# Kernel optimization log

Hardware: AMD Instinct MI355X
Metric: run time of the kernel (lower is better)

## Reference

```python
import jax, jax.numpy as jnp
import numpy as np

N = 50000; E = 800000; NFEAT = 128; NHID = 64; CONCAT = 2; NCLASS = 40
D = CONCAT * NHID
BN_EPS = 1e-5


def setup_inputs() -> dict:
    key = jax.random.key(0)
    ks = jax.random.split(key, 16)
    rn = lambda k, s, sc=0.05: jax.random.normal(k, s, jnp.float32) * sc
    return {
        "x1a": rn(ks[0], (N, NFEAT), 1.0),
        "x1b": rn(ks[1], (N, NFEAT), 1.0),
        "x2a": rn(ks[2], (N, NFEAT), 1.0),
        "x2b": rn(ks[3], (N, NFEAT), 1.0),
        "edge_index1": jax.random.randint(ks[4], (2, E), 0, N),
        "edge_index2": jax.random.randint(ks[5], (2, E), 0, N),
        "Wi": rn(ks[6], (CONCAT, NFEAT, NHID)),
        "bi": jnp.zeros((CONCAT, NHID), jnp.float32),
        "gi": jnp.ones((CONCAT, NHID), jnp.float32),
        "bei": jnp.zeros((CONCAT, NHID), jnp.float32),
        "Wm": rn(ks[7], (2, D, D)),
        "bm": jnp.zeros((2, D), jnp.float32),
        "gm": jnp.ones((2, D), jnp.float32),
        "bem": jnp.zeros((2, D), jnp.float32),
        "Wf": rn(ks[8], (D, NCLASS)),
        "bf": jnp.zeros((NCLASS,), jnp.float32),
        "fc1w1_W": rn(ks[9], (D,)),
        "fc1w1_b": jnp.zeros((1,), jnp.float32),
        "fc1w2_W": rn(ks[10], (D,)),
        "fc1w2_b": jnp.zeros((1,), jnp.float32),
        "aws_w1_W": rn(ks[11], (2, D)),
        "aws_w1_b": jnp.zeros((2,), jnp.float32),
        "aws_w2_W": rn(ks[12], (2, D)),
        "aws_w2_b": jnp.zeros((2,), jnp.float32),
        "fcw1_W": rn(ks[13], (NCLASS,)),
        "fcw1_b": jnp.zeros((1,), jnp.float32),
        "fcw2_W": rn(ks[14], (NCLASS,)),
        "fcw2_b": jnp.zeros((1,), jnp.float32),
    }


def _gcn_norm(edge_index, n):
    # GCN symmetric normalization with self-loops (cached=True behaviour)
    loop = jnp.arange(n)
    src = jnp.concatenate([edge_index[0], loop])
    dst = jnp.concatenate([edge_index[1], loop])
    deg = jax.ops.segment_sum(jnp.ones_like(dst, jnp.float32), dst, n)
    dinv = jnp.where(deg > 0, deg ** -0.5, 0.0)
    return src, dst, dinv[src] * dinv[dst]


def _gcn(x, W, b, g):
    # GCNConv: dense projection then sparse scatter-based aggregation
    src, dst, norm = g
    h = x @ W
    agg = jax.ops.segment_sum(h[src] * norm[:, None], dst, x.shape[0])
    return agg + b


def _bn(x, gamma, beta):
    m = x.mean(0)
    v = jnp.mean((x - m) ** 2, axis=0)
    return (x - m) * jax.lax.rsqrt(v + BN_EPS) * gamma + beta


def _gate(x1, x2, w1, b1, w2, b2):
    # sigmoid gates L1-normalized; only the last node's row is used (w[-1,:])
    s1 = jax.nn.sigmoid(jnp.dot(x1[-1], w1) + b1)
    s2 = jax.nn.sigmoid(jnp.dot(x2[-1], w2) + b2)
    t = s1 + s2
    return s1 / t, s2 / t


def _forward(x1a, x1b, x2a, x2b, g1, g2, Wi, bi, gi, bei, Wm, bm, gm, bem,
             Wf, bf, fc1w1_W, fc1w1_b, fc1w2_W, fc1w2_b,
             aws_w1_W, aws_w1_b, aws_w2_W, aws_w2_b,
             fcw1_W, fcw1_b, fcw2_W, fcw2_b):
    xs1, xs2 = (x1a, x1b), (x2a, x2b)
    h1 = jnp.concatenate([jax.nn.relu(_bn(_gcn(xs1[i], Wi[i], bi[i], g1), gi[i], bei[i]))
                          for i in range(CONCAT)], axis=-1)
    h2 = jnp.concatenate([jax.nn.relu(_bn(_gcn(xs2[i], Wi[i], bi[i], g2), gi[i], bei[i]))
                          for i in range(CONCAT)], axis=-1)
    w1, w2 = _gate(h1, h2, fc1w1_W, fc1w1_b[0], fc1w2_W, fc1w2_b[0])
    x = w1 * h1 + w2 * h2
    for i in range(Wm.shape[0]):  # middle layers (n_layers - 2)
        a = jax.nn.relu(_bn(_gcn(x, Wm[i], bm[i], g1), gm[i], bem[i]))
        b = jax.nn.relu(_bn(_gcn(x, Wm[i], bm[i], g2), gm[i], bem[i]))
        w1, w2 = _gate(a, b, aws_w1_W[i], aws_w1_b[i], aws_w2_W[i], aws_w2_b[i])
        x = w1 * a + w2 * b
    p1 = _gcn(x, Wf, bf, g1)
    p2 = _gcn(x, Wf, bf, g2)
    w1, w2 = _gate(p1, p2, fcw1_W, fcw1_b[0], fcw2_W, fcw2_b[0])
    return (w1 * p1 + w2 * p2, p1, p2)


def reference(x1a, x1b, x2a, x2b, edge_index1, edge_index2, Wi, bi, gi, bei,
              Wm, bm, gm, bem, Wf, bf, fc1w1_W, fc1w1_b, fc1w2_W, fc1w2_b,
              aws_w1_W, aws_w1_b, aws_w2_W, aws_w2_b,
              fcw1_W, fcw1_b, fcw2_W, fcw2_b):
    g1 = _gcn_norm(edge_index1, N)
    g2 = _gcn_norm(edge_index2, N)
    return _forward(x1a, x1b, x2a, x2b, g1, g2, Wi, bi, gi, bei, Wm, bm, gm, bem,
                    Wf, bf, fc1w1_W, fc1w1_b, fc1w2_W, fc1w2_b,
                    aws_w1_W, aws_w1_b, aws_w2_W, aws_w2_b,
                    fcw1_W, fcw1_b, fcw2_W, fcw2_b)
```

## Files before the change

### kernel.cpp

```cpp
#include <hip/hip_runtime.h>
#include <hip/hip_fp16.h>


#define DFEAT 128

typedef __attribute__((ext_vector_type(8))) short bf16x8;
typedef __attribute__((ext_vector_type(4))) float f32x4;

__device__ __forceinline__ unsigned short f2bf(float f) {
    unsigned u = __float_as_uint(f);
    u += 0x7fffu + ((u >> 16) & 1u);
    return (unsigned short)(u >> 16);
}
__device__ __forceinline__ float bf2f(unsigned short u) {
    return __uint_as_float((unsigned)u << 16);
}
__device__ __forceinline__ float4 bf4tof4(ushort4 u) {
    return make_float4(__uint_as_float((unsigned)u.x << 16),
                       __uint_as_float((unsigned)u.y << 16),
                       __uint_as_float((unsigned)u.z << 16),
                       __uint_as_float((unsigned)u.w << 16));
}
__device__ __forceinline__ unsigned f2h16(float f) {
    return (unsigned)__half_as_ushort(__float2half(f));
}
__device__ __forceinline__ float h16f(unsigned u) {
    return __half2float(__ushort_as_half((unsigned short)u));
}

constexpr int RSH = 13;
constexpr int RSZ = 8192;
constexpr int NRMAX = 8;
constexpr int EPA = 2048;
constexpr int SUBS = 16;
constexpr int SCAP = 160000;

__global__ __launch_bounds__(256) void partA_kernel(
    const int* __restrict__ src1, const int* __restrict__ dst1,
    const int* __restrict__ src2, const int* __restrict__ dst2,
    int* __restrict__ stg, int* __restrict__ gcount, int E, int nr) {
    int g = blockIdx.y;
    const int* src = g ? src2 : src1;
    const int* dst = g ? dst2 : dst1;
    __shared__ int buf[EPA];
    __shared__ int buf2[EPA];
    __shared__ int cnt8[NRMAX + 1], pre8[NRMAX + 1], base8[NRMAX];
    int t = threadIdx.x;
    if (t < NRMAX) cnt8[t] = 0;
    __syncthreads();
    int e0 = blockIdx.x * EPA;
    int e1 = min(e0 + EPA, E);
    int ec = e1 - e0;
    for (int i = e0 + t; i < e1; i += 256) {
        int d = dst[i];
        int s = src[i];
        buf[i - e0] = (d << 16) | s;
        atomicAdd(&cnt8[d >> RSH], 1);
    }
    __syncthreads();
    if (t == 0) {
        int run = 0;
        for (int r = 0; r < nr; ++r) { pre8[r] = run; run += cnt8[r]; }
        pre8[nr] = run;
    }
    __syncthreads();
    if (t < nr) {
        base8[t] = atomicAdd(&gcount[g * NRMAX + t], cnt8[t]);
        cnt8[t] = 0;
    }
    __syncthreads();
    for (int j = t; j < ec; j += 256) {
        int v = buf[j];
        int d = (unsigned)v >> 16;
        int r = d >> RSH;
        int p = pre8[r] + atomicAdd(&cnt8[r], 1);
        buf2[p] = ((d & (RSZ - 1)) << 16) | (v & 0xFFFF);
    }
    __syncthreads();
    for (int j = t; j < ec; j += 256) {
        int r = 0;
        while (j >= pre8[r + 1]) ++r;
        int gpos = base8[r] + (j - pre8[r]);
        if (gpos < SCAP) stg[((size_t)g * NRMAX + r) * SCAP + gpos] = buf2[j];
    }
}

__global__ __launch_bounds__(256) void histB_kernel(
    const int* __restrict__ stg, const int* __restrict__ gcount,
    int* __restrict__ baseB, int nr) {
    int g = blockIdx.y;
    int r = blockIdx.x / SUBS;
    int sub = blockIdx.x % SUBS;
    __shared__ int hist[RSZ];
    int t = threadIdx.x;
    for (int i = t; i < RSZ; i += 256) hist[i] = 0;
    __syncthreads();
    int len = min(gcount[g * NRMAX + r], SCAP);
    int seg = (len + SUBS - 1) / SUBS;
    int e0 = sub * seg, e1 = min(e0 + seg, len);
    const int* sp = stg + ((size_t)g * NRMAX + r) * SCAP;
    for (int i = e0 + t; i < e1; i += 256) atomicAdd(&hist[(unsigned)sp[i] >> 16], 1);
    __syncthreads();
    int* bp = baseB + (((size_t)(g * NRMAX + r) * SUBS + sub) << RSH);
    for (int i = t; i < RSZ; i += 256) bp[i] = hist[i];
}

__global__ __launch_bounds__(256) void scanB_kernel(
    int* __restrict__ baseB, int* __restrict__ cnt1, int* __restrict__ cnt2, int n) {
    int node = blockIdx.x * 256 + threadIdx.x;
    int g = blockIdx.y;
    if (node >= n) return;
    int r = node >> RSH, dloc = node & (RSZ - 1);
    int* p = baseB + (((size_t)(g * NRMAX + r) * SUBS) << RSH) + dloc;
    int run = 0;
#pragma unroll
    for (int s = 0; s < SUBS; ++s) {
        int v = p[(size_t)s << RSH];
        p[(size_t)s << RSH] = run;
        run += v;
    }
    (g ? cnt2 : cnt1)[node] = run;
}

__global__ __launch_bounds__(256) void fillC_kernel(
    const int* __restrict__ stg, const int* __restrict__ gcount,
    const int* __restrict__ baseB,
    const int* __restrict__ rp1, const int* __restrict__ rp2,
    const float* __restrict__ dv1, const float* __restrict__ dv2,
    int* __restrict__ cs1, int* __restrict__ cs2, int n, int nr) {
    int g = blockIdx.y;
    int r = blockIdx.x / SUBS;
    int sub = blockIdx.x % SUBS;
    const int* rp = g ? rp2 : rp1;
    const float* dv = g ? dv2 : dv1;
    int* cs = g ? cs2 : cs1;
    __shared__ int off[RSZ];
    int t = threadIdx.x;
    int r0 = r << RSH;
    int rn = min(RSZ, n - r0);
    if (rn <= 0) return;
    const int* bp = baseB + (((size_t)(g * NRMAX + r) * SUBS + sub) << RSH);
    for (int i = t; i < rn; i += 256) off[i] = bp[i] + rp[r0 + i];
    __syncthreads();
    int len = min(gcount[g * NRMAX + r], SCAP);
    int seg = (len + SUBS - 1) / SUBS;
    int e0 = sub * seg, e1 = min(e0 + seg, len);
    const int* sp = stg + ((size_t)g * NRMAX + r) * SCAP;
    for (int i = e0 + t; i < e1; i += 256) {
        int v = sp[i];
        int dloc = (unsigned)v >> 16;
        int s = v & 0xFFFF;
        float w = dv[r0 + dloc] * dv[s];
        int pos = atomicAdd(&off[dloc], 1);
        cs[pos] = (int)((f2h16(w) << 16) | (unsigned)s);
    }
}

__global__ __launch_bounds__(256) void blocksum_kernel(const int* __restrict__ c1,
                                                       const int* __restrict__ c2,
                                                       int* __restrict__ bs, int n, int nb) {
    const int* c = blockIdx.y ? c2 : c1;
    int* out = bs + (size_t)blockIdx.y * nb;
    int t = threadIdx.x;
    int base = blockIdx.x * 2048 + t * 8;
    int s = 0;
#pragma unroll
    for (int i = 0; i < 8; ++i) {
        int idx = base + i;
        if (idx < n) s += c[idx];
    }
    __shared__ int red[256];
    red[t] = s;
    __syncthreads();
    for (int o = 128; o > 0; o >>= 1) {
        if (t < o) red[t] += red[t + o];
        __syncthreads();
    }
    if (t == 0) out[blockIdx.x] = red[0];
}

__global__ void scansums_kernel(int* __restrict__ bs, int nb, int* __restrict__ rp1,
                                int* __restrict__ rp2, int n, int E, float* __restrict__ stats) {
    int t = threadIdx.x;
    if (t < 2) {
        int* b = bs + (size_t)t * nb;
        int run = 0;
        for (int i = 0; i < nb; ++i) {
            int v = b[i];
            b[i] = run;
            run += v;
        }
        (t ? rp2 : rp1)[n] = E;
    }
    for (int i = t; i < 512; i += 64) stats[i] = 0.f;
}

__global__ __launch_bounds__(256) void writerp_kernel(const int* __restrict__ c1,
                                                      const int* __restrict__ c2,
                                                      const int* __restrict__ bs,
                                                      int* __restrict__ rp1, int* __restrict__ rp2,
                                                      float* __restrict__ dv1,
                                                      float* __restrict__ dv2, int n, int nb) {
    const int* c = blockIdx.y ? c2 : c1;
    int* rp = blockIdx.y ? rp2 : rp1;
    float* dv = blockIdx.y ? dv2 : dv1;
    int boff = bs[(size_t)blockIdx.y * nb + blockIdx.x];
    int t = threadIdx.x;
    int base = blockIdx.x * 2048 + t * 8;
    int v[8];
    int s = 0;
#pragma unroll
    for (int i = 0; i < 8; ++i) {
        int idx = base + i;
        v[i] = (idx < n) ? c[idx] : 0;
        s += v[i];
    }
    __shared__ int red[256];
    red[t] = s;
    __syncthreads();
    for (int o = 1; o < 256; o <<= 1) {
        int x = (t >= o) ? red[t - o] : 0;
        __syncthreads();
        red[t] += x;
        __syncthreads();
    }
    int run = boff + red[t] - s;
#pragma unroll
    for (int i = 0; i < 8; ++i) {
        int idx = base + i;
        if (idx < n) {
            rp[idx] = run;
            dv[idx] = rsqrtf((float)(v[i] + 1));
            run += v[i];
        }
    }
}

template <int FV, typename OutT>
__global__ __launch_bounds__(256) void dualagg_kernel(
    const unsigned short* __restrict__ h1, const unsigned short* __restrict__ h2,
    const int* __restrict__ rp1, const int* __restrict__ cs1, const float* __restrict__ dv1,
    const int* __restrict__ rp2, const int* __restrict__ cs2, const float* __restrict__ dv2,
    const float* __restrict__ bias, OutT* __restrict__ o1, OutT* __restrict__ o2, int n) {
    constexpr int COLS = FV * 4;
    const unsigned short* h;
    const int *rp, *cs;
    const float* dv;
    OutT* out;
    if (blockIdx.y == 0) { h = h1; rp = rp1; cs = cs1; dv = dv1; out = o1; }
    else                 { h = h2; rp = rp2; cs = cs2; dv = dv2; out = o2; }
    int wid = blockIdx.x * 4 + (threadIdx.x >> 6);
    if (wid >= n) return;
    int lane = threadIdx.x & 63;
    int half = lane >> 5;
    int l = lane & 31;
    bool act = (l < FV);
    float4 acc = make_float4(0.f, 0.f, 0.f, 0.f);
    int e0 = rp[wid], e1 = rp[wid + 1];
    int e = e0 + half;
    for (; e + 6 < e1; e += 8) {
        int va = cs[e], vb = cs[e + 2], vc = cs[e + 4], vd = cs[e + 6];
        float wa = h16f((unsigned)va >> 16); int sa = va & 0xFFFF;
        float wb = h16f((unsigned)vb >> 16); int sb = vb & 0xFFFF;
        float wc = h16f((unsigned)vc >> 16); int sc = vc & 0xFFFF;
        float wd = h16f((unsigned)vd >> 16); int sd = vd & 0xFFFF;
        if (act) {
            float4 ha = bf4tof4(((const ushort4*)(h + (size_t)sa * COLS))[l]);
            float4 hb = bf4tof4(((const ushort4*)(h + (size_t)sb * COLS))[l]);
            float4 hc = bf4tof4(((const ushort4*)(h + (size_t)sc * COLS))[l]);
            float4 hd = bf4tof4(((const ushort4*)(h + (size_t)sd * COLS))[l]);
            acc.x = fmaf(wa, ha.x, acc.x); acc.y = fmaf(wa, ha.y, acc.y);
            acc.z = fmaf(wa, ha.z, acc.z); acc.w = fmaf(wa, ha.w, acc.w);
            acc.x = fmaf(wb, hb.x, acc.x); acc.y = fmaf(wb, hb.y, acc.y);
            acc.z = fmaf(wb, hb.z, acc.z); acc.w = fmaf(wb, hb.w, acc.w);
            acc.x = fmaf(wc, hc.x, acc.x); acc.y = fmaf(wc, hc.y, acc.y);
            acc.z = fmaf(wc, hc.z, acc.z); acc.w = fmaf(wc, hc.w, acc.w);
            acc.x = fmaf(wd, hd.x, acc.x); acc.y = fmaf(wd, hd.y, acc.y);
            acc.z = fmaf(wd, hd.z, acc.z); acc.w = fmaf(wd, hd.w, acc.w);
        }
    }
    for (; e < e1; e += 2) {
        int va = cs[e];
        float wa = h16f((unsigned)va >> 16); int sa = va & 0xFFFF;
        if (act) {
            float4 ha = bf4tof4(((const ushort4*)(h + (size_t)sa * COLS))[l]);
            acc.x = fmaf(wa, ha.x, acc.x); acc.y = fmaf(wa, ha.y, acc.y);
            acc.z = fmaf(wa, ha.z, acc.z); acc.w = fmaf(wa, ha.w, acc.w);
        }
    }
    acc.x += __shfl_xor(acc.x, 32);
    acc.y += __shfl_xor(acc.y, 32);
    acc.z += __shfl_xor(acc.z, 32);
    acc.w += __shfl_xor(acc.w, 32);
    if (half == 0 && act) {
        float dn = dv[wid];
        float w = dn * dn;
        float4 hv = bf4tof4(((const ushort4*)(h + (size_t)wid * COLS))[l]);
        acc.x = fmaf(w, hv.x, acc.x); acc.y = fmaf(w, hv.y, acc.y);
        acc.z = fmaf(w, hv.z, acc.z); acc.w = fmaf(w, hv.w, acc.w);
        float4 b = ((const float4*)bias)[l];
        acc.x += b.x; acc.y += b.y; acc.z += b.z; acc.w += b.w;
        if constexpr (sizeof(OutT) == 4) {
            ((float4*)((float*)out + (size_t)wid * COLS))[l] = acc;
        } else {
            ushort4 o;
            o.x = f2bf(acc.x); o.y = f2bf(acc.y); o.z = f2bf(acc.z); o.w = f2bf(acc.w);
            ((ushort4*)((unsigned short*)out + (size_t)wid * COLS))[l] = o;
        }
    }
}

__global__ __launch_bounds__(256) void gemm_l1_kernel(
    const float* __restrict__ x1a, const float* __restrict__ x1b, const float* __restrict__ x2a,
    const float* __restrict__ x2b, const float* __restrict__ Wi, unsigned short* __restrict__ H1,
    unsigned short* __restrict__ H2, int nrows) {
    constexpr int CG = 16;
    const float* X = (blockIdx.y == 0) ? x1a : (blockIdx.y == 1) ? x1b
                     : (blockIdx.y == 2) ? x2a : x2b;
    const float* W = Wi + (blockIdx.y & 1) * 128 * 64;
    unsigned short* Y = (blockIdx.y < 2) ? H1 : H2;
    int ocol = (int)(blockIdx.y & 1) * 64;
    __shared__ float Ws[32][64];
    __shared__ float Xs[64][32];
    int tid = threadIdx.x;
    int row0 = blockIdx.x * 64;
    int cg = tid % CG;
    int rg = tid / CG;
    float4 acc[4];
#pragma unroll
    for (int i = 0; i < 4; ++i) acc[i] = make_float4(0.f, 0.f, 0.f, 0.f);
    for (int kc = 0; kc < 4; ++kc) {
        for (int i = tid; i < 32 * CG; i += 256) {
            int r = i / CG, c = i % CG;
            *(float4*)&Ws[r][c * 4] = *(const float4*)(W + (size_t)(kc * 32 + r) * 64 + c * 4);
        }
        for (int i = tid; i < 64 * 8; i += 256) {
            int r = i / 8, c = i % 8;
            int gr = row0 + r;
            float4 v = make_float4(0.f, 0.f, 0.f, 0.f);
            if (gr < nrows) v = *(const float4*)(X + (size_t)gr * DFEAT + kc * 32 + c * 4);
            *(float4*)&Xs[r][c * 4] = v;
        }
        __syncthreads();
#pragma unroll
        for (int k = 0; k < 32; ++k) {
            float4 w = *(float4*)&Ws[k][cg * 4];
#pragma unroll
            for (int i = 0; i < 4; ++i) {
                float a = Xs[rg * 4 + i][k];
                acc[i].x = fmaf(a, w.x, acc[i].x);
                acc[i].y = fmaf(a, w.y, acc[i].y);
                acc[i].z = fmaf(a, w.z, acc[i].z);
                acc[i].w = fmaf(a, w.w, acc[i].w);
            }
        }
        __syncthreads();
    }
#pragma unroll
    for (int i = 0; i < 4; ++i) {
        int r = row0 + rg * 4 + i;
        if (r < nrows) {
            ushort4 o;
            o.x = f2bf(acc[i].x); o.y = f2bf(acc[i].y);
            o.z = f2bf(acc[i].z); o.w = f2bf(acc[i].w);
            *(ushort4*)(Y + (size_t)r * DFEAT + ocol + cg * 4) = o;
        }
    }
}

__global__ __launch_bounds__(256) void prepW_kernel(const float* __restrict__ Wm,
                                                    unsigned short* __restrict__ Wt) {
    int o = blockIdx.x * 256 + threadIdx.x;
    int l = blockIdx.y;
    int kk = o & 31;
    int col = (o >> 5) & 127;
    int kc = o >> 12;
    int k = kc * 32 + kk;
    Wt[(size_t)l * 16384 + o] = f2bf(Wm[(size_t)l * 16384 + (size_t)k * 128 + col]);
}

__global__ __launch_bounds__(256) void gemm_mfma_kernel(
    const unsigned short* __restrict__ Abf, const unsigned short* __restrict__ Bbf,
    const float* __restrict__ ss, const float* __restrict__ wout,
    const unsigned short* __restrict__ Wt, unsigned short* __restrict__ Y, int nrows) {
    __shared__ short Xs[64][128];
    int tid = threadIdx.x;
    int row0 = blockIdx.x * 64;
    int wave = tid >> 6, lane = tid & 63;
    int m = lane & 15, quad = lane >> 4;
    float w1 = wout[0], w2 = wout[1];
    for (int u = tid; u < 1024; u += 256) {
        int r = u >> 4;
        int col0 = (u & 15) * 8;
        int gr = row0 + r;
        if (gr < nrows) {
#pragma unroll
            for (int hh = 0; hh < 2; ++hh) {
                int c = col0 + hh * 4;
                float4 fa = bf4tof4(*(const ushort4*)(Abf + (size_t)gr * 128 + c));
                float4 fb = bf4tof4(*(const ushort4*)(Bbf + (size_t)gr * 128 + c));
                float4 sa = *(const float4*)(ss + c);
                float4 ha = *(const float4*)(ss + 128 + c);
                float4 sb = *(const float4*)(ss + 256 + c);
                float4 hb = *(const float4*)(ss + 384 + c);
                ushort4 o;
                o.x = f2bf(w1 * fmaxf(fmaf(fa.x, sa.x, ha.x), 0.f) +
                           w2 * fmaxf(fmaf(fb.x, sb.x, hb.x), 0.f));
                o.y = f2bf(w1 * fmaxf(fmaf(fa.y, sa.y, ha.y), 0.f) +
                           w2 * fmaxf(fmaf(fb.y, sb.y, hb.y), 0.f));
                o.z = f2bf(w1 * fmaxf(fmaf(fa.z, sa.z, ha.z), 0.f) +
                           w2 * fmaxf(fmaf(fb.z, sb.z, hb.z), 0.f));
                o.w = f2bf(w1 * fmaxf(fmaf(fa.w, sa.w, ha.w), 0.f) +
                           w2 * fmaxf(fmaf(fb.w, sb.w, hb.w), 0.f));
                *(ushort4*)&Xs[r][c] = o;
            }
        } else {
            ushort4 z = {0, 0, 0, 0};
            *(ushort4*)&Xs[r][col0] = z;
            *(ushort4*)&Xs[r][col0 + 4] = z;
        }
    }
    __syncthreads();
    f32x4 acc[8];
#pragma unroll
    for (int i = 0; i < 8; ++i) acc[i] = (f32x4){0.f, 0.f, 0.f, 0.f};
#pragma unroll
    for (int kc = 0; kc < 4; ++kc) {
        bf16x8 a = *(const bf16x8*)&Xs[wave * 16 + m][kc * 32 + quad * 8];
#pragma unroll
        for (int ct = 0; ct < 8; ++ct) {
            const short* bp = (const short*)(Wt + ((size_t)(kc * 128 + ct * 16 + m) * 32) + quad * 8);
            bf16x8 b = *(const bf16x8*)bp;
            acc[ct] = __builtin_amdgcn_mfma_f32_16x16x32_bf16(a, b, acc[ct], 0, 0, 0);
        }
    }
#pragma unroll
    for (int ct = 0; ct < 8; ++ct) {
#pragma unroll
        for (int i = 0; i < 4; ++i) {
            int gr = row0 + wave * 16 + quad * 4 + i;
            if (gr < nrows) Y[(size_t)gr * 128 + ct * 16 + m] = f2bf(acc[ct][i]);
        }
    }
}

template <int CG, int RPT>
__global__ __launch_bounds__(256) void gemm_fused_kernel(
    const unsigned short* __restrict__ Abf, const unsigned short* __restrict__ Bbf,
    const float* __restrict__ ss, const float* __restrict__ wout, const float* __restrict__ W,
    unsigned short* __restrict__ Y, int nrows, int fout, int ostride) {
    __shared__ float Ws[32][CG * 4];
    __shared__ float Xs[64][32];
    int tid = threadIdx.x;
    int row0 = blockIdx.x * 64;
    int cg = tid % CG;
    int rg = tid / CG;
    float w1 = wout[0], w2 = wout[1];
    float4 acc[RPT];
#pragma unroll
    for (int i = 0; i < RPT; ++i) acc[i] = make_float4(0.f, 0.f, 0.f, 0.f);
    for (int kc = 0; kc < 4; ++kc) {
        for (int i = tid; i < 32 * CG; i += 256) {
            int r = i / CG, c = i % CG;
            float4 w;
            if ((c * 4 + 3) < fout) {
                w = *(const float4*)(W + (size_t)(kc * 32 + r) * fout + c * 4);
            } else {
                float t0 = (c * 4 + 0) < fout ? W[(size_t)(kc * 32 + r) * fout + c * 4 + 0] : 0.f;
                float t1 = (c * 4 + 1) < fout ? W[(size_t)(kc * 32 + r) * fout + c * 4 + 1] : 0.f;
                float t2 = (c * 4 + 2) < fout ? W[(size_t)(kc * 32 + r) * fout + c * 4 + 2] : 0.f;
                float t3 = (c * 4 + 3) < fout ? W[(size_t)(kc * 32 + r) * fout + c * 4 + 3] : 0.f;
                w = make_float4(t0, t1, t2, t3);
            }
            *(float4*)&Ws[r][c * 4] = w;
        }
        for (int i = tid; i < 64 * 8; i += 256) {
            int r = i / 8, c = i % 8;
            int gr = row0 + r;
            int col0 = kc * 32 + c * 4;
            float4 v = make_float4(0.f, 0.f, 0.f, 0.f);
            if (gr < nrows) {
                float4 a = bf4tof4(*(const ushort4*)(Abf + (size_t)gr * DFEAT + col0));
                float4 b = bf4tof4(*(const ushort4*)(Bbf + (size_t)gr * DFEAT + col0));
                float4 scA = *(const float4*)(ss + col0);
                float4 shA = *(const float4*)(ss + DFEAT + col0);
                float4 scB = *(const float4*)(ss + 2 * DFEAT + col0);
                float4 shB = *(const float4*)(ss + 3 * DFEAT + col0);
                v.x = w1 * fmaxf(fmaf(a.x, scA.x, shA.x), 0.f) +
                      w2 * fmaxf(fmaf(b.x, scB.x, shB.x), 0.f);
                v.y = w1 * fmaxf(fmaf(a.y, scA.y, shA.y), 0.f) +
                      w2 * fmaxf(fmaf(b.y, scB.y, shB.y), 0.f);
                v.z = w1 * fmaxf(fmaf(a.z, scA.z, shA.z), 0.f) +
                      w2 * fmaxf(fmaf(b.z, scB.z, shB.z), 0.f);
                v.w = w1 * fmaxf(fmaf(a.w, scA.w, shA.w), 0.f) +
                      w2 * fmaxf(fmaf(b.w, scB.w, shB.w), 0.f);
            }
            *(float4*)&Xs[r][c * 4] = v;
        }
        __syncthreads();
#pragma unroll
        for (int k = 0; k < 32; ++k) {
            float4 w = *(float4*)&Ws[k][cg * 4];
#pragma unroll
            for (int i = 0; i < RPT; ++i) {
                float a = Xs[rg * RPT + i][k];
                acc[i].x = fmaf(a, w.x, acc[i].x);
                acc[i].y = fmaf(a, w.y, acc[i].y);
                acc[i].z = fmaf(a, w.z, acc[i].z);
                acc[i].w = fmaf(a, w.w, acc[i].w);
            }
        }
        __syncthreads();
    }
    if (cg * 4 < fout) {
#pragma unroll
        for (int i = 0; i < RPT; ++i) {
            int r = row0 + rg * RPT + i;
            if (r < nrows) {
                ushort4 o;
                o.x = f2bf(acc[i].x); o.y = f2bf(acc[i].y);
                o.z = f2bf(acc[i].z); o.w = f2bf(acc[i].w);
                *(ushort4*)(Y + (size_t)r * ostride + cg * 4) = o;
            }
        }
    }
}

__global__ __launch_bounds__(256) void stats2_kernel(const unsigned short* __restrict__ A,
                                                     const unsigned short* __restrict__ B,
                                                     float* __restrict__ stats, int nrows) {
    __shared__ float red1[256];
    __shared__ float red2[256];
    int t = threadIdx.x;
    int col = t & 127;
    int rg = t >> 7;
    const unsigned short* src = (blockIdx.y == 0) ? A : B;
    float* st = stats + (size_t)blockIdx.y * 256;
    int r0 = blockIdx.x * 128 + rg * 64;
    int r1 = min(r0 + 64, nrows);
    float s = 0.f, s2 = 0.f;
    for (int r = r0; r < r1; ++r) {
        float v = bf2f(src[(size_t)r * DFEAT + col]);
        s += v;
        s2 = fmaf(v, v, s2);
    }
    red1[t] = s;
    red2[t] = s2;
    __syncthreads();
    if (t < 128) {
        atomicAdd(&st[col], red1[t] + red1[t + 128]);
        atomicAdd(&st[DFEAT + col], red2[t] + red2[t + 128]);
    }
}

__global__ __launch_bounds__(128) void gate_prep_kernel(
    float* __restrict__ statsA, float* __restrict__ statsB,
    const unsigned short* __restrict__ preA, const unsigned short* __restrict__ preB,
    const float* __restrict__ gamma, const float* __restrict__ beta,
    const float* __restrict__ gwA, const float* __restrict__ gbA,
    const float* __restrict__ gwB, const float* __restrict__ gbB,
    float* __restrict__ ss, float* __restrict__ wout, int nrows) {
    __shared__ float red[128];
    __shared__ float dotA_s;
    int t = threadIdx.x;
    float invN = 1.f / (float)nrows;
    float meanA = statsA[t] * invN;
    float varA = statsA[DFEAT + t] * invN - meanA * meanA;
    float scA = gamma[t] * rsqrtf(varA + 1e-5f);
    float shA = beta[t] - meanA * scA;
    ss[t] = scA;
    ss[DFEAT + t] = shA;
    float meanB = statsB[t] * invN;
    float varB = statsB[DFEAT + t] * invN - meanB * meanB;
    float scB = gamma[t] * rsqrtf(varB + 1e-5f);
    float shB = beta[t] - meanB * scB;
    ss[2 * DFEAT + t] = scB;
    ss[3 * DFEAT + t] = shB;
    statsA[t] = 0.f;
    statsA[DFEAT + t] = 0.f;
    statsB[t] = 0.f;
    statsB[DFEAT + t] = 0.f;
    float av = fmaxf(fmaf(bf2f(preA[(size_t)(nrows - 1) * DFEAT + t]), scA, shA), 0.f);
    red[t] = av * gwA[t];
    __syncthreads();
    for (int s = 64; s > 0; s >>= 1) {
        if (t < s) red[t] += red[t + s];
        __syncthreads();
    }
    if (t == 0) dotA_s = red[0];
    __syncthreads();
    float bv = fmaxf(fmaf(bf2f(preB[(size_t)(nrows - 1) * DFEAT + t]), scB, shB), 0.f);
    red[t] = bv * gwB[t];
    __syncthreads();
    for (int s = 64; s > 0; s >>= 1) {
        if (t < s) red[t] += red[t + s];
        __syncthreads();
    }
    if (t == 0) {
        float s1 = 1.f / (1.f + expf(-(dotA_s + gbA[0])));
        float s2 = 1.f / (1.f + expf(-(red[0] + gbB[0])));
        float tt = s1 + s2;
        wout[0] = s1 / tt;
        wout[1] = s2 / tt;
    }
}

__global__ __launch_bounds__(64) void gate_final_kernel(
    const float* __restrict__ p1, const float* __restrict__ p2,
    const float* __restrict__ w1v, const float* __restrict__ b1,
    const float* __restrict__ w2v, const float* __restrict__ b2,
    float* __restrict__ wout, int nrows, int nclass) {
    __shared__ float red[64];
    __shared__ float dot1_s;
    int t = threadIdx.x;
    float v = (t < nclass) ? p1[(size_t)(nrows - 1) * nclass + t] * w1v[t] : 0.f;
    red[t] = v;
    __syncthreads();
    for (int s = 32; s > 0; s >>= 1) {
        if (t < s) red[t] += red[t + s];
        __syncthreads();
    }
    if (t == 0) dot1_s = red[0];
    __syncthreads();
    v = (t < nclass) ? p2[(size_t)(nrows - 1) * nclass + t] * w2v[t] : 0.f;
    red[t] = v;
    __syncthreads();
    for (int s = 32; s > 0; s >>= 1) {
        if (t < s) red[t] += red[t + s];
        __syncthreads();
    }
    if (t == 0) {
        float s1 = 1.f / (1.f + expf(-(dot1_s + b1[0])));
        float s2 = 1.f / (1.f + expf(-(red[0] + b2[0])));
        float tt = s1 + s2;
        wout[0] = s1 / tt;
        wout[1] = s2 / tt;
    }
}

__global__ __launch_bounds__(256) void mix_kernel(const float* __restrict__ p1,
                                                  const float* __restrict__ p2,
                                                  const float* __restrict__ wout,
                                                  float* __restrict__ o, int n4) {
    int idx = blockIdx.x * blockDim.x + threadIdx.x;
    if (idx >= n4) return;
    float w1 = wout[0], w2 = wout[1];
    float4 a = *(const float4*)(p1 + (size_t)idx * 4);
    float4 b = *(const float4*)(p2 + (size_t)idx * 4);
    float4 r = make_float4(w1 * a.x + w2 * b.x, w1 * a.y + w2 * b.y, w1 * a.z + w2 * b.z,
                           w1 * a.w + w2 * b.w);
    *(float4*)(o + (size_t)idx * 4) = r;
}

extern "C" void kernel_launch(void* const* d_in, const int* in_sizes, int n_in, void* d_out,
                              int out_size, void* d_ws, size_t ws_size, hipStream_t stream) {
    (void)n_in; (void)out_size; (void)ws_size;
    const int N = in_sizes[0] / DFEAT;
    const int E = in_sizes[4] / 2;
    const int NC = in_sizes[15];

    const float* x1a = (const float*)d_in[0];
    const float* x1b = (const float*)d_in[1];
    const float* x2a = (const float*)d_in[2];
    const float* x2b = (const float*)d_in[3];
    const int* ei1 = (const int*)d_in[4];
    const int* ei2 = (const int*)d_in[5];
    const float* Wi = (const float*)d_in[6];
    const float* bi = (const float*)d_in[7];
    const float* gi = (const float*)d_in[8];
    const float* bei = (const float*)d_in[9];
    const float* Wm = (const float*)d_in[10];
    const float* bm = (const float*)d_in[11];
    const float* gm = (const float*)d_in[12];
    const float* bem = (const float*)d_in[13];
    const float* Wf = (const float*)d_in[14];
    const float* bf = (const float*)d_in[15];
    const float* fc1w1_W = (const float*)d_in[16];
    const float* fc1w1_b = (const float*)d_in[17];
    const float* fc1w2_W = (const float*)d_in[18];
    const float* fc1w2_b = (const float*)d_in[19];
    const float* aws_w1_W = (const float*)d_in[20];
    const float* aws_w1_b = (const float*)d_in[21];
    const float* aws_w2_W = (const float*)d_in[22];
    const float* aws_w2_b = (const float*)d_in[23];
    const float* fcw1_W = (const float*)d_in[24];
    const float* fcw1_b = (const float*)d_in[25];
    const float* fcw2_W = (const float*)d_in[26];
    const float* fcw2_b = (const float*)d_in[27];

    char* ws = (char*)d_ws;
    size_t off = 0;
    auto alloc = [&](size_t bytes) -> char* {
        char* p = ws + off;
        off += (bytes + 255) & ~(size_t)255;
        return p;
    };
    unsigned short* A = (unsigned short*)alloc((size_t)N * DFEAT * 2);
    unsigned short* B = (unsigned short*)alloc((size_t)N * DFEAT * 2);
    unsigned short* H1 = (unsigned short*)alloc((size_t)N * DFEAT * 2);
    unsigned short* H2 = (unsigned short*)alloc((size_t)N * DFEAT * 2);
    int* rp1 = (int*)alloc((size_t)(N + 1) * 4);
    int* rp2 = (int*)alloc((size_t)(N + 1) * 4);
    int* cnt1 = (int*)alloc((size_t)N * 4);
    int* cnt2 = (int*)alloc((size_t)N * 4);
    float* dv1 = (float*)alloc((size_t)N * 4);
    float* dv2 = (float*)alloc((size_t)N * 4);
    int* cs1 = (int*)alloc((size_t)E * 4);
    int* cs2 = (int*)alloc((size_t)E * 4);
    int* stg = (int*)alloc((size_t)2 * NRMAX * SCAP * 4);
    int* baseB = (int*)alloc(((size_t)2 * NRMAX * SUBS << RSH) * 4);
    int* gcount = (int*)alloc(2 * NRMAX * 4);
    unsigned short* Wt = (unsigned short*)alloc((size_t)2 * 16384 * 2);
    float* stats = (float*)alloc(2048);
    float* statsA = stats;
    float* statsB = stats + 256;
    float* ssbuf = (float*)alloc(2048);
    float* wout = (float*)alloc(256);
    int nb = (N + 2047) / 2048;
    int* bsums = (int*)alloc((size_t)2 * nb * 4);

    const int* src1 = ei1;
    const int* dst1 = ei1 + E;
    const int* src2 = ei2;
    const int* dst2 = ei2 + E;

    int nr = (N + RSZ - 1) >> RSH;
    int gemmbl = (N + 63) / 64;
    dim3 pagrid((E + EPA - 1) / EPA, 2);
    dim3 rsgrid(nr * SUBS, 2);
    dim3 ssgrid((N + 255) / 256, 2);
    dim3 agggrid((N + 3) / 4, 2);
    dim3 statgrid((N + 127) / 128, 2);
    dim3 scangrid(nb, 2);
    dim3 l1grid(gemmbl, 4);
    dim3 prepgrid(64, 2);

    hipMemsetAsync(gcount, 0, 2 * NRMAX * 4, stream);
    prepW_kernel<<<prepgrid, 256, 0, stream>>>(Wm, Wt);
    partA_kernel<<<pagrid, 256, 0, stream>>>(src1, dst1, src2, dst2, stg, gcount, E, nr);
    histB_kernel<<<rsgrid, 256, 0, stream>>>(stg, gcount, baseB, nr);
    scanB_kernel<<<ssgrid, 256, 0, stream>>>(baseB, cnt1, cnt2, N);
    blocksum_kernel<<<scangrid, 256, 0, stream>>>(cnt1, cnt2, bsums, N, nb);
    scansums_kernel<<<1, 64, 0, stream>>>(bsums, nb, rp1, rp2, N, E, stats);
    writerp_kernel<<<scangrid, 256, 0, stream>>>(cnt1, cnt2, bsums, rp1, rp2, dv1, dv2, N, nb);
    fillC_kernel<<<rsgrid, 256, 0, stream>>>(stg, gcount, baseB, rp1, rp2, dv1, dv2,
                                             cs1, cs2, N, nr);

    gemm_l1_kernel<<<l1grid, 256, 0, stream>>>(x1a, x1b, x2a, x2b, Wi, H1, H2, N);
    dualagg_kernel<32, unsigned short><<<agggrid, 256, 0, stream>>>(
        H1, H2, rp1, cs1, dv1, rp2, cs2, dv2, bi, A, B, N);
    stats2_kernel<<<statgrid, 256, 0, stream>>>(A, B, stats, N);
    gate_prep_kernel<<<1, 128, 0, stream>>>(statsA, statsB, A, B, gi, bei, fc1w1_W, fc1w1_b,
                                            fc1w2_W, fc1w2_b, ssbuf, wout, N);

    gemm_mfma_kernel<<<gemmbl, 256, 0, stream>>>(A, B, ssbuf, wout, Wt, H1, N);
    dualagg_kernel<32, unsigned short><<<agggrid, 256, 0, stream>>>(
        H1, H1, rp1, cs1, dv1, rp2, cs2, dv2, bm, A, B, N);
    stats2_kernel<<<statgrid, 256, 0, stream>>>(A, B, stats, N);
    gate_prep_kernel<<<1, 128, 0, stream>>>(statsA, statsB, A, B, gm, bem, aws_w1_W, aws_w1_b,
                                            aws_w2_W, aws_w2_b, ssbuf, wout, N);

    gemm_mfma_kernel<<<gemmbl, 256, 0, stream>>>(A, B, ssbuf, wout, Wt + 16384, H1, N);
    dualagg_kernel<32, unsigned short><<<agggrid, 256, 0, stream>>>(
        H1, H1, rp1, cs1, dv1, rp2, cs2, dv2, bm + 128, A, B, N);
    stats2_kernel<<<statgrid, 256, 0, stream>>>(A, B, stats, N);
    gate_prep_kernel<<<1, 128, 0, stream>>>(statsA, statsB, A, B, gm + 128, bem + 128,
                                            aws_w1_W + 128, aws_w1_b + 1, aws_w2_W + 128,
                                            aws_w2_b + 1, ssbuf, wout, N);

    float* out0 = (float*)d_out;
    float* p1 = out0 + (size_t)N * NC;
    float* p2 = out0 + (size_t)2 * N * NC;
    gemm_fused_kernel<16, 4><<<gemmbl, 256, 0, stream>>>(A, B, ssbuf, wout, Wf, H2, N, NC, NC);
    dualagg_kernel<10, float><<<agggrid, 256, 0, stream>>>(H2, H2, rp1, cs1, dv1, rp2, cs2, dv2,
                                                           bf, p1, p2, N);
    gate_final_kernel<<<1, 64, 0, stream>>>(p1, p2, fcw1_W, fcw1_b, fcw2_W, fcw2_b, wout, N, NC);
    mix_kernel<<<(N * NC / 4 + 255) / 256, 256, 0, stream>>>(p1, p2, wout, out0, N * NC / 4);
}
```

Before: 688.6 us.

## Use split-bf16 MFMA for first-layer GEMM and swizzle LDS tiles

Replaces the FP32 FMA first-layer projection with MFMA bf16 matrix instructions, splitting both the activations and the weights into high and low bf16 parts and issuing three MFMAs per tile to keep near-fp32 accuracy. A new prep kernel pre-splits and re-lays out Wi. LDS tiles in both MFMA GEMMs now use an XOR swizzle to avoid bank conflicts, and the fused FP32 GEMM pads its Xs tile to 33 columns. The three-pass split adds MFMA work and an extra launch in exchange for moving the projection off the vector ALUs.

New measurement: 694.0 us. No clear change (+0.8%).

```diff
diff --git a/kernel.cpp b/kernel.cpp
--- a/kernel.cpp
+++ b/kernel.cpp
@@ -310,60 +310,91 @@
     }
 }
 
+__global__ __launch_bounds__(256) void prepW1_kernel(const float* __restrict__ Wi,
+                                                     unsigned short* __restrict__ Wt1) {
+    int o = blockIdx.x * 256 + threadIdx.x;
+    int kk = o & 31;
+    int col = (o >> 5) & 63;
+    int kc = (o >> 11) & 3;
+    int h = (o >> 13) & 1;
+    int s = (o >> 14) & 1;
+    float w = Wi[(size_t)s * 8192 + (size_t)(kc * 32 + kk) * 64 + col];
+    unsigned short hi = f2bf(w);
+    Wt1[o] = h ? f2bf(w - bf2f(hi)) : hi;
+}
+
 __global__ __launch_bounds__(256) void gemm_l1_kernel(
     const float* __restrict__ x1a, const float* __restrict__ x1b, const float* __restrict__ x2a,
-    const float* __restrict__ x2b, const float* __restrict__ Wi, unsigned short* __restrict__ H1,
-    unsigned short* __restrict__ H2, int nrows) {
-    constexpr int CG = 16;
+    const float* __restrict__ x2b, const unsigned short* __restrict__ Wt1,
+    unsigned short* __restrict__ H1, unsigned short* __restrict__ H2, int nrows) {
     const float* X = (blockIdx.y == 0) ? x1a : (blockIdx.y == 1) ? x1b
                      : (blockIdx.y == 2) ? x2a : x2b;
-    const float* W = Wi + (blockIdx.y & 1) * 128 * 64;
+    int slice = blockIdx.y & 1;
     unsigned short* Y = (blockIdx.y < 2) ? H1 : H2;
-    int ocol = (int)(blockIdx.y & 1) * 64;
-    __shared__ float Ws[32][64];
-    __shared__ float Xs[64][32];
+    int ocol = slice * 64;
+    __shared__ unsigned short Xh[64 * 128];
+    __shared__ unsigned short Xl[64 * 128];
     int tid = threadIdx.x;
     int row0 = blockIdx.x * 64;
-    int cg = tid % CG;
-    int rg = tid / CG;
-    float4 acc[4];
-#pragma unroll
-    for (int i = 0; i < 4; ++i) acc[i] = make_float4(0.f, 0.f, 0.f, 0.f);
+    int wave = tid >> 6, lane = tid & 63;
+    int m = lane & 15, quad = lane >> 4;
+    for (int u = tid; u < 1024; u += 256) {
+        int r = u >> 4;
+        int c8 = (u & 15) * 8;
+        int sc = c8 ^ ((r & 7) << 3);
+        int gr = row0 + r;
+        ushort4 h0, h1v, l0, l1v;
+        if (gr < nrows) {
+            float4 f0 = *(const float4*)(X + (size_t)gr * DFEAT + c8);
+            float4 f1 = *(const float4*)(X + (size_t)gr * DFEAT + c8 + 4);
+            float fs[8] = {f0.x, f0.y, f0.z, f0.w, f1.x, f1.y, f1.z, f1.w};
+            unsigned short hv[8], lv[8];
+#pragma unroll
+            for (int j = 0; j < 8; ++j) {
+                unsigned short hh = f2bf(fs[j]);
+                hv[j] = hh;
+                lv[j] = f2bf(fs[j] - bf2f(hh));
+            }
+            h0 = make_ushort4(hv[0], hv[1], hv[2], hv[3]);
+            h1v = make_ushort4(hv[4], hv[5], hv[6], hv[7]);
+            l0 = make_ushort4(lv[0], lv[1], lv[2], lv[3]);
+            l1v = make_ushort4(lv[4], lv[5], lv[6], lv[7]);
+        } else {
+            h0 = h1v = l0 = l1v = make_ushort4(0, 0, 0, 0);
+        }
+        *(ushort4*)&Xh[r * 128 + sc] = h0;
+        *(ushort4*)&Xh[r * 128 + sc + 4] = h1v;
+        *(ushort4*)&Xl[r * 128 + sc] = l0;
+        *(ushort4*)&Xl[r * 128 + sc + 4] = l1v;
+    }
+    __syncthreads();
+    f32x4 acc[4];
+#pragma unroll
+    for (int i = 0; i < 4; ++i) acc[i] = (f32x4){0.f, 0.f, 0.f, 0.f};
+    int arow = wave * 16 + m;
+    const unsigned short* Whp = Wt1 + (size_t)slice * 16384;
+    const unsigned short* Wlp = Whp + 8192;
+#pragma unroll
     for (int kc = 0; kc < 4; ++kc) {
-        for (int i = tid; i < 32 * CG; i += 256) {
-            int r = i / CG, c = i % CG;
-            *(float4*)&Ws[r][c * 4] = *(const float4*)(W + (size_t)(kc * 32 + r) * 64 + c * 4);
-        }
-        for (int i = tid; i < 64 * 8; i += 256) {
-            int r = i / 8, c = i % 8;
-            int gr = row0 + r;
-            float4 v = make_float4(0.f, 0.f, 0.f, 0.f);
-            if (gr < nrows) v = *(const float4*)(X + (size_t)gr * DFEAT + kc * 32 + c * 4);
-            *(float4*)&Xs[r][c * 4] = v;
-        }
-        __syncthreads();
-#pragma unroll
-        for (int k = 0; k < 32; ++k) {
-            float4 w = *(float4*)&Ws[k][cg * 4];
-#pragma unroll
-            for (int i = 0; i < 4; ++i) {
-                float a = Xs[rg * 4 + i][k];
-                acc[i].x = fmaf(a, w.x, acc[i].x);
-                acc[i].y = fmaf(a, w.y, acc[i].y);
-                acc[i].z = fmaf(a, w.z, acc[i].z);
-                acc[i].w = fmaf(a, w.w, acc[i].w);
-            }
-        }
-        __syncthreads();
-    }
-#pragma unroll
-    for (int i = 0; i < 4; ++i) {
-        int r = row0 + rg * 4 + i;
-        if (r < nrows) {
-            ushort4 o;
-            o.x = f2bf(acc[i].x); o.y = f2bf(acc[i].y);
-            o.z = f2bf(acc[i].z); o.w = f2bf(acc[i].w);
-            *(ushort4*)(Y + (size_t)r * DFEAT + ocol + cg * 4) = o;
+        int ac = (kc * 32 + quad * 8) ^ ((arow & 7) << 3);
+        bf16x8 ah = *(const bf16x8*)&Xh[arow * 128 + ac];
+        bf16x8 al = *(const bf16x8*)&Xl[arow * 128 + ac];
+#pragma unroll
+        for (int ct = 0; ct < 4; ++ct) {
+            int wo = kc * 2048 + (ct * 16 + m) * 32 + quad * 8;
+            bf16x8 bh = *(const bf16x8*)(Whp + wo);
+            bf16x8 bl = *(const bf16x8*)(Wlp + wo);
+            acc[ct] = __builtin_amdgcn_mfma_f32_16x16x32_bf16(ah, bh, acc[ct], 0, 0, 0);
+            acc[ct] = __builtin_amdgcn_mfma_f32_16x16x32_bf16(al, bh, acc[ct], 0, 0, 0);
+            acc[ct] = __builtin_amdgcn_mfma_f32_16x16x32_bf16(ah, bl, acc[ct], 0, 0, 0);
+        }
+    }
+#pragma unroll
+    for (int ct = 0; ct < 4; ++ct) {
+#pragma unroll
+        for (int i = 0; i < 4; ++i) {
+            int gr = row0 + wave * 16 + quad * 4 + i;
+            if (gr < nrows) Y[(size_t)gr * DFEAT + ocol + ct * 16 + m] = f2bf(acc[ct][i]);
         }
     }
 }
@@ -383,7 +414,7 @@
     const unsigned short* __restrict__ Abf, const unsigned short* __restrict__ Bbf,
     const float* __restrict__ ss, const float* __restrict__ wout,
     const unsigned short* __restrict__ Wt, unsigned short* __restrict__ Y, int nrows) {
-    __shared__ short Xs[64][128];
+    __shared__ unsigned short Xs[64 * 128];
     int tid = threadIdx.x;
     int row0 = blockIdx.x * 64;
     int wave = tid >> 6, lane = tid & 63;
@@ -393,6 +424,7 @@
         int r = u >> 4;
         int col0 = (u & 15) * 8;
         int gr = row0 + r;
+        int swz = (r & 7) << 3;
         if (gr < nrows) {
 #pragma unroll
             for (int hh = 0; hh < 2; ++hh) {
@@ -412,24 +444,26 @@
                            w2 * fmaxf(fmaf(fb.z, sb.z, hb.z), 0.f));
                 o.w = f2bf(w1 * fmaxf(fmaf(fa.w, sa.w, ha.w), 0.f) +
                            w2 * fmaxf(fmaf(fb.w, sb.w, hb.w), 0.f));
-                *(ushort4*)&Xs[r][c] = o;
+                *(ushort4*)&Xs[r * 128 + (c ^ swz)] = o;
             }
         } else {
             ushort4 z = {0, 0, 0, 0};
-            *(ushort4*)&Xs[r][col0] = z;
-            *(ushort4*)&Xs[r][col0 + 4] = z;
+            *(ushort4*)&Xs[r * 128 + (col0 ^ swz)] = z;
+            *(ushort4*)&Xs[r * 128 + ((col0 + 4) ^ swz)] = z;
         }
     }
     __syncthreads();
     f32x4 acc[8];
 #pragma unroll
     for (int i = 0; i < 8; ++i) acc[i] = (f32x4){0.f, 0.f, 0.f, 0.f};
+    int arow = wave * 16 + m;
 #pragma unroll
     for (int kc = 0; kc < 4; ++kc) {
-        bf16x8 a = *(const bf16x8*)&Xs[wave * 16 + m][kc * 32 + quad * 8];
+        int ac = (kc * 32 + quad * 8) ^ ((arow & 7) << 3);
+        bf16x8 a = *(const bf16x8*)&Xs[arow * 128 + ac];
 #pragma unroll
         for (int ct = 0; ct < 8; ++ct) {
-            const short* bp = (const short*)(Wt + ((size_t)(kc * 128 + ct * 16 + m) * 32) + quad * 8);
+            const unsigned short* bp = Wt + ((size_t)(kc * 128 + ct * 16 + m) * 32) + quad * 8;
             bf16x8 b = *(const bf16x8*)bp;
             acc[ct] = __builtin_amdgcn_mfma_f32_16x16x32_bf16(a, b, acc[ct], 0, 0, 0);
         }
@@ -450,7 +484,7 @@
     const float* __restrict__ ss, const float* __restrict__ wout, const float* __restrict__ W,
     unsigned short* __restrict__ Y, int nrows, int fout, int ostride) {
     __shared__ float Ws[32][CG * 4];
-    __shared__ float Xs[64][32];
+    __shared__ float Xs[64][33];
     int tid = threadIdx.x;
     int row0 = blockIdx.x * 64;
     int cg = tid % CG;
@@ -495,7 +529,10 @@
                 v.w = w1 * fmaxf(fmaf(a.w, scA.w, shA.w), 0.f) +
                       w2 * fmaxf(fmaf(b.w, scB.w, shB.w), 0.f);
             }
-            *(float4*)&Xs[r][c * 4] = v;
+            Xs[r][c * 4 + 0] = v.x;
+            Xs[r][c * 4 + 1] = v.y;
+            Xs[r][c * 4 + 2] = v.z;
+            Xs[r][c * 4 + 3] = v.w;
         }
         __syncthreads();
 #pragma unroll
@@ -711,6 +748,7 @@
     int* baseB = (int*)alloc(((size_t)2 * NRMAX * SUBS << RSH) * 4);
     int* gcount = (int*)alloc(2 * NRMAX * 4);
     unsigned short* Wt = (unsigned short*)alloc((size_t)2 * 16384 * 2);
+    unsigned short* Wt1 = (unsigned short*)alloc((size_t)32768 * 2);
     float* stats = (float*)alloc(2048);
     float* statsA = stats;
     float* statsB = stats + 256;
@@ -737,6 +775,7 @@
 
     hipMemsetAsync(gcount, 0, 2 * NRMAX * 4, stream);
     prepW_kernel<<<prepgrid, 256, 0, stream>>>(Wm, Wt);
+    prepW1_kernel<<<128, 256, 0, stream>>>(Wi, Wt1);
     partA_kernel<<<pagrid, 256, 0, stream>>>(src1, dst1, src2, dst2, stg, gcount, E, nr);
     histB_kernel<<<rsgrid, 256, 0, stream>>>(stg, gcount, baseB, nr);
     scanB_kernel<<<ssgrid, 256, 0, stream>>>(baseB, cnt1, cnt2, N);
@@ -746,7 +785,7 @@
     fillC_kernel<<<rsgrid, 256, 0, stream>>>(stg, gcount, baseB, rp1, rp2, dv1, dv2,
                                              cs1, cs2, N, nr);
 
-    gemm_l1_kernel<<<l1grid, 256, 0, stream>>>(x1a, x1b, x2a, x2b, Wi, H1, H2, N);
+    gemm_l1_kernel<<<l1grid, 256, 0, stream>>>(x1a, x1b, x2a, x2b, Wt1, H1, H2, N);
     dualagg_kernel<32, unsigned short><<<agggrid, 256, 0, stream>>>(
         H1, H2, rp1, cs1, dv1, rp2, cs2, dv2, bi, A, B, N);
     stats2_kernel<<<statgrid, 256, 0, stream>>>(A, B, stats, N);
```
